# Optimization experiments

Hardware: AMD Instinct MI355X
Metric: run time of the kernel (lower is better)

Reference implementation:

```python
import jax, jax.numpy as jnp
import numpy as np

N = 500_000          # num nodes
K = 3                # neighbors per star subgraph = graphlet_size - 1
E = N * K            # one subgraph per node -> directed (center, nbr) edges
L = 2                # hop_neighbor
FD = 2               # final_dim = 2**pqc_dim
H = 64               # hidden_dim
NC = 8               # num_classes
NIN = 16             # node_input_dim
EIN = 8              # edge_input_dim


def _lin(k, i, o):
    # torch.nn.Linear-style init scale
    return jax.random.normal(k, (i, o), jnp.float32) * (1.0 / np.sqrt(i))


def setup_inputs() -> dict:
    key = jax.random.key(0)
    ks = jax.random.split(key, 32)
    node_feat = jax.random.normal(ks[0], (N, NIN), jnp.float32)
    edge_attr = jax.random.normal(ks[1], (E, EIN), jnp.float32)
    # edge e = (center, neighbor); centers grouped: edges 3i..3i+2 belong to node i
    centers = jnp.repeat(jnp.arange(N, dtype=jnp.int32), K)
    neighbors = jax.random.randint(ks[2], (E,), 0, N, dtype=jnp.int32)
    edge_index = jnp.stack([centers, neighbors])  # [2, E]
    batch = jnp.zeros((N,), jnp.int32)
    msg_W1 = jnp.stack([_lin(ks[6 + i], 2 * FD, H) for i in range(L)])
    msg_W2 = jnp.stack([_lin(ks[8 + i], H, FD) for i in range(L)])
    upd_W1 = jnp.stack([_lin(ks[10 + i], 2 * FD, H) for i in range(L)])
    upd_W2 = jnp.stack([_lin(ks[12 + i], H, FD) for i in range(L)])
    return dict(
        node_feat=node_feat, edge_attr=edge_attr, edge_index=edge_index, batch=batch,
        Wn=_lin(ks[3], NIN, FD), bn=jnp.zeros((FD,), jnp.float32),
        We=_lin(ks[4], EIN, FD), be=jnp.zeros((FD,), jnp.float32),
        msg_W1=msg_W1, msg_b1=jnp.zeros((L, H), jnp.float32),
        msg_W2=msg_W2, msg_b2=jnp.zeros((L, FD), jnp.float32),
        upd_W1=upd_W1, upd_b1=jnp.zeros((L, H), jnp.float32),
        upd_W2=upd_W2, upd_b2=jnp.zeros((L, FD), jnp.float32),
        fin_W1=_lin(ks[14], FD, H), fin_b1=jnp.zeros((H,), jnp.float32),
        fin_W2=_lin(ks[15], H, NC), fin_b2=jnp.zeros((NC,), jnp.float32),
    )


def _leaky(x):
    return jnp.where(x >= 0, x, 0.1 * x)


def _mlp(x, W1, b1, W2, b2):
    # MLP([din, 64, dout], act=LeakyReLU(0.1)); dropout inactive at eval
    return _leaky(x @ W1 + b1) @ W2 + b2


def reference(node_feat, edge_attr, edge_index, batch, Wn, bn, We, be,
              msg_W1, msg_b1, msg_W2, msg_b2, upd_W1, upd_b1, upd_W2, upd_b2,
              fin_W1, fin_b1, fin_W2, fin_b2):
    ctr = edge_index[0]  # [E] center of each star edge
    nbr = edge_index[1]  # [E] neighbor
    h = node_feat @ Wn + bn      # [N, FD] input_node projection
    e = edge_attr @ We + be      # [E, FD] input_edge projection (fixed across layers)
    for l in range(L):
        # message over each (center, neighbor) edge: concat(edge_feat, nbr_feat)
        msg = _mlp(jnp.concatenate([e, h[nbr]], axis=1),
                   msg_W1[l], msg_b1[l], msg_W2[l], msg_b2[l])  # [E, FD]
        aggr = jax.ops.segment_sum(msg, ctr, num_segments=N)    # [N, FD]
        new = _mlp(jnp.concatenate([h, aggr], axis=1),
                   upd_W1[l], upd_b1[l], upd_W2[l], upd_b2[l])  # [N, FD]
        h = jax.nn.relu(h + new)  # updates_node[center] += new_center; then ReLU
    return _mlp(h, fin_W1, fin_b1, fin_W2, fin_b2)  # [N, NC]
```

## Files before the change

### kernel.cpp

```cpp
#include <hip/hip_runtime.h>

#define NN 500000
#define HALF 250000
#define KK 3
#define EE (NN * KK)
#define HH 64
#define NC 8
#define NIN 16
#define EIN 8

typedef __attribute__((ext_vector_type(2))) _Float16 h2;
typedef __attribute__((ext_vector_type(2)))  float sf2;
typedef __attribute__((ext_vector_type(8)))  float sf8;
typedef __attribute__((ext_vector_type(16))) float sf16;

using pk_t = decltype(__builtin_amdgcn_cvt_pkrtz(0.f, 0.f));

__device__ __forceinline__ sf2 sload2(const float* p) {
    sf2 r; asm("s_load_dwordx2 %0, %1, 0x0" : "=s"(r) : "s"(p)); return r;
}
__device__ __forceinline__ sf8 sload8(const float* p) {
    sf8 r; asm("s_load_dwordx8 %0, %1, 0x0" : "=s"(r) : "s"(p)); return r;
}
__device__ __forceinline__ sf16 sload16(const float* p) {
    sf16 r; asm("s_load_dwordx16 %0, %1, 0x0" : "=s"(r) : "s"(p)); return r;
}
#define SWAIT1(a)         asm volatile("s_waitcnt lgkmcnt(0)" : "+s"(a))
#define SWAIT2(a,b)       asm volatile("s_waitcnt lgkmcnt(0)" : "+s"(a),"+s"(b))
#define SWAIT3(a,b,c)     asm volatile("s_waitcnt lgkmcnt(0)" : "+s"(a),"+s"(b),"+s"(c))
#define SWAIT4(a,b,c,d)   asm volatile("s_waitcnt lgkmcnt(0)" : "+s"(a),"+s"(b),"+s"(c),"+s"(d))
#define SWAIT5(a,b,c,d,e) asm volatile("s_waitcnt lgkmcnt(0)" : "+s"(a),"+s"(b),"+s"(c),"+s"(d),"+s"(e))

#if __has_builtin(__builtin_elementwise_fma)
#define PKFMA(a,b,c) __builtin_elementwise_fma((a),(b),(c))
#else
#define PKFMA(a,b,c) ((a)*(b)+(c))
#endif

__device__ __forceinline__ h2 bch2(float f)        { return __builtin_bit_cast(h2, f); }
__device__ __forceinline__ h2 bch2u(unsigned int u){ return __builtin_bit_cast(h2, u); }
__device__ __forceinline__ h2 dup16(float f) {
    return __builtin_bit_cast(h2, __builtin_amdgcn_cvt_pkrtz(f, f));
}
__device__ __forceinline__ unsigned int pkrtz_u(float a, float b) {
    return __builtin_bit_cast(unsigned int, __builtin_amdgcn_cvt_pkrtz(a, b));
}
__device__ __forceinline__ h2 splat_lo(unsigned int u) {
    h2 p = bch2u(u); h2 r; r.x = p.x; r.y = p.x; return r;
}
__device__ __forceinline__ h2 splat_hi(unsigned int u) {
    h2 p = bch2u(u); h2 r; r.x = p.y; r.y = p.y; return r;
}
__device__ __forceinline__ float lo_f32(unsigned int u) { return (float)bch2u(u).x; }
__device__ __forceinline__ float hi_f32(unsigned int u) { return (float)bch2u(u).y; }

__device__ __forceinline__ float fdot2(h2 a, h2 b, float c) {
#if __has_builtin(__builtin_amdgcn_fdot2)
    return __builtin_amdgcn_fdot2(__builtin_bit_cast(pk_t, a),
                                  __builtin_bit_cast(pk_t, b), c, false);
#else
    return c + (float)a.x * (float)b.x + (float)a.y * (float)b.y;
#endif
}
__device__ __forceinline__ h2 lk2(h2 x) {
    h2 c = {(_Float16)0.1f, (_Float16)0.1f};
    return __builtin_elementwise_max(x, x * c);
}
__device__ __forceinline__ float pack2(float a, float b) {
    h2 v; v.x = (_Float16)a; v.y = (_Float16)b;
    return __builtin_bit_cast(float, v);
}

__global__ __launch_bounds__(256) void prep_kernel(
    const float* __restrict__ node_feat, const float* __restrict__ edge_attr,
    const float* __restrict__ Wn, const float* __restrict__ bn,
    const float* __restrict__ We, const float* __restrict__ be,
    unsigned int* __restrict__ hp, unsigned int* __restrict__ ep,
    const float* __restrict__ msgW1, const float* __restrict__ msgb1, const float* __restrict__ msgW2,
    const float* __restrict__ updW1, const float* __restrict__ updb1, const float* __restrict__ updW2,
    const float* __restrict__ finW1, const float* __restrict__ finb1, const float* __restrict__ finW2,
    float* __restrict__ wpack)
{
    sf16 wn0 = sload16(Wn);
    sf16 wn1 = sload16(Wn + 16);
    sf2  bnv = sload2(bn);
    sf16 wev = sload16(We);
    sf2  bev = sload2(be);
    SWAIT5(wn0, wn1, bnv, wev, bev);

    int idx = blockIdx.x * 256 + threadIdx.x;
    if (idx < NN) {
        const float4* x4 = (const float4*)(node_feat + (size_t)idx * NIN);
        float4 v0 = x4[0], v1 = x4[1], v2 = x4[2], v3 = x4[3];
        float xs[16] = {v0.x, v0.y, v0.z, v0.w, v1.x, v1.y, v1.z, v1.w,
                        v2.x, v2.y, v2.z, v2.w, v3.x, v3.y, v3.z, v3.w};
        float a0 = bnv.x, a1 = bnv.y;
#pragma unroll
        for (int i = 0; i < 8; i++) {
            a0 = fmaf(xs[i], wn0[2 * i], a0);
            a1 = fmaf(xs[i], wn0[2 * i + 1], a1);
        }
#pragma unroll
        for (int i = 0; i < 8; i++) {
            a0 = fmaf(xs[8 + i], wn1[2 * i], a0);
            a1 = fmaf(xs[8 + i], wn1[2 * i + 1], a1);
        }
        hp[idx] = pkrtz_u(a0, a1);
    } else if (idx < NN + EE) {
        int eidx = idx - NN;
        const float4* x4 = (const float4*)(edge_attr + (size_t)eidx * EIN);
        float4 v0 = x4[0], v1 = x4[1];
        float xs[8] = {v0.x, v0.y, v0.z, v0.w, v1.x, v1.y, v1.z, v1.w};
        float a0 = bev.x, a1 = bev.y;
#pragma unroll
        for (int i = 0; i < 8; i++) {
            a0 = fmaf(xs[i], wev[2 * i], a0);
            a1 = fmaf(xs[i], wev[2 * i + 1], a1);
        }
        ep[eidx] = pkrtz_u(a0, a1);
    }

    if (blockIdx.x == 0) {
        int t = threadIdx.x;
        if (t < 32) {
            int l = t >> 4, which = (t >> 3) & 1, c = t & 7;
            const float* W1 = (which ? updW1 : msgW1) + l * 4 * HH;
            const float* b1 = (which ? updb1 : msgb1) + l * HH;
            const float* W2 = (which ? updW2 : msgW2) + l * 2 * HH;
            float* dst = wpack + (l * 2 + which) * 256 + c * 32;
            int j0 = c * 8;
            for (int r = 0; r < 4; r++)
                for (int p = 0; p < 4; p++)
                    dst[r * 4 + p] = pack2(W1[r * HH + j0 + 2 * p], W1[r * HH + j0 + 2 * p + 1]);
            for (int p = 0; p < 4; p++) {
                dst[16 + p] = pack2(b1[j0 + 2 * p], b1[j0 + 2 * p + 1]);
                dst[20 + p] = pack2(W2[(j0 + 2 * p) * 2 + 0], W2[(j0 + 2 * p + 1) * 2 + 0]);
                dst[24 + p] = pack2(W2[(j0 + 2 * p) * 2 + 1], W2[(j0 + 2 * p + 1) * 2 + 1]);
                dst[28 + p] = 0.0f;
            }
        } else if (t < 40) {
            int c = t - 32, j0 = c * 8;
            float* dst = wpack + 1024 + c * 48;
            for (int p = 0; p < 4; p++) {
                dst[p]      = pack2(finW1[j0 + 2 * p],      finW1[j0 + 2 * p + 1]);
                dst[4 + p]  = pack2(finW1[HH + j0 + 2 * p], finW1[HH + j0 + 2 * p + 1]);
                dst[8 + p]  = pack2(finb1[j0 + 2 * p],      finb1[j0 + 2 * p + 1]);
                dst[12 + p] = 0.0f;
            }
            for (int jp = 0; jp < 4; jp++)
                for (int cc = 0; cc < NC; cc++)
                    dst[16 + jp * 8 + cc] = pack2(finW2[(j0 + 2 * jp) * NC + cc],
                                                  finW2[(j0 + 2 * jp + 1) * NC + cc]);
        }
    }
}

template<bool FINAL>
__global__ __launch_bounds__(256) void layer_kernel(
    const unsigned int* __restrict__ hp_in, const unsigned int* __restrict__ eP,
    const int* __restrict__ nbr,
    const float* __restrict__ mblk, const float* __restrict__ mb2,
    const float* __restrict__ ublk, const float* __restrict__ ub2,
    unsigned int* __restrict__ hp_out,
    const float* __restrict__ fblk, const float* __restrict__ fb2,
    float* __restrict__ out)
{
    int tA = blockIdx.x * 256 + threadIdx.x;
    if (tA >= HALF) return;
    int iA = tA, iB = tA + HALF;

    sf2 mb2v = sload2(mb2);
    sf2 ub2v = sload2(ub2);
    SWAIT2(mb2v, ub2v);

    unsigned int hA = hp_in[iA], hB = hp_in[iB];
    int baseA = iA * KK, baseB = iB * KK;
    int nA0 = nbr[baseA], nA1 = nbr[baseA + 1], nA2 = nbr[baseA + 2];
    int nB0 = nbr[baseB], nB1 = nbr[baseB + 1], nB2 = nbr[baseB + 2];
    unsigned int gA0 = hp_in[nA0], gA1 = hp_in[nA1], gA2 = hp_in[nA2];
    unsigned int gB0 = hp_in[nB0], gB1 = hp_in[nB1], gB2 = hp_in[nB2];
    unsigned int eA0 = eP[baseA], eA1 = eP[baseA + 1], eA2 = eP[baseA + 2];
    unsigned int eB0 = eP[baseB], eB1 = eP[baseB + 1], eB2 = eP[baseB + 2];

    h2 eA0x = splat_lo(eA0), eA0y = splat_hi(eA0);
    h2 eA1x = splat_lo(eA1), eA1y = splat_hi(eA1);
    h2 eA2x = splat_lo(eA2), eA2y = splat_hi(eA2);
    h2 eB0x = splat_lo(eB0), eB0y = splat_hi(eB0);
    h2 eB1x = splat_lo(eB1), eB1y = splat_hi(eB1);
    h2 eB2x = splat_lo(eB2), eB2y = splat_hi(eB2);
    h2 nA0x = splat_lo(gA0), nA0y = splat_hi(gA0);
    h2 nA1x = splat_lo(gA1), nA1y = splat_hi(gA1);
    h2 nA2x = splat_lo(gA2), nA2y = splat_hi(gA2);
    h2 nB0x = splat_lo(gB0), nB0y = splat_hi(gB0);
    h2 nB1x = splat_lo(gB1), nB1y = splat_hi(gB1);
    h2 nB2x = splat_lo(gB2), nB2y = splat_hi(gB2);

    float a0A = 3.0f * mb2v.x, a1A = 3.0f * mb2v.y;
    float a0B = a0A, a1B = a1A;
#pragma unroll 1
    for (int c = 0; c < 8; c += 2) {
        sf16 A0 = sload16(mblk + c * 32);
        sf16 B0 = sload16(mblk + c * 32 + 16);
        sf16 A1 = sload16(mblk + c * 32 + 32);
        sf16 B1 = sload16(mblk + c * 32 + 48);
        SWAIT4(A0, B0, A1, B1);
#pragma unroll
        for (int half = 0; half < 2; half++) {
            const sf16& A = half ? A1 : A0;
            const sf16& B = half ? B1 : B0;
#pragma unroll
            for (int jp = 0; jp < 4; jp++) {
                h2 w0 = bch2(A[jp]), w1 = bch2(A[4 + jp]);
                h2 w2 = bch2(A[8 + jp]), w3 = bch2(A[12 + jp]);
                h2 bb = bch2(B[jp]);
                h2 wcx = bch2(B[4 + jp]), wcy = bch2(B[8 + jp]);
                h2 t0 = PKFMA(eA0x, w0, PKFMA(eA0y, w1, PKFMA(nA0x, w2, PKFMA(nA0y, w3, bb))));
                h2 t1 = PKFMA(eA1x, w0, PKFMA(eA1y, w1, PKFMA(nA1x, w2, PKFMA(nA1y, w3, bb))));
                h2 t2 = PKFMA(eA2x, w0, PKFMA(eA2y, w1, PKFMA(nA2x, w2, PKFMA(nA2y, w3, bb))));
                h2 tsA = lk2(t0) + lk2(t1) + lk2(t2);
                a0A = fdot2(tsA, wcx, a0A);
                a1A = fdot2(tsA, wcy, a1A);
                h2 s0 = PKFMA(eB0x, w0, PKFMA(eB0y, w1, PKFMA(nB0x, w2, PKFMA(nB0y, w3, bb))));
                h2 s1 = PKFMA(eB1x, w0, PKFMA(eB1y, w1, PKFMA(nB1x, w2, PKFMA(nB1y, w3, bb))));
                h2 s2 = PKFMA(eB2x, w0, PKFMA(eB2y, w1, PKFMA(nB2x, w2, PKFMA(nB2y, w3, bb))));
                h2 tsB = lk2(s0) + lk2(s1) + lk2(s2);
                a0B = fdot2(tsB, wcx, a0B);
                a1B = fdot2(tsB, wcy, a1B);
            }
        }
    }

    h2 hAx = splat_lo(hA), hAy = splat_hi(hA);
    h2 hBx = splat_lo(hB), hBy = splat_hi(hB);
    h2 aAx = dup16(a0A), aAy = dup16(a1A);
    h2 aBx = dup16(a0B), aBy = dup16(a1B);
    float u0A = ub2v.x, u1A = ub2v.y, u0B = ub2v.x, u1B = ub2v.y;
#pragma unroll 1
    for (int c = 0; c < 8; c += 2) {
        sf16 A0 = sload16(ublk + c * 32);
        sf16 B0 = sload16(ublk + c * 32 + 16);
        sf16 A1 = sload16(ublk + c * 32 + 32);
        sf16 B1 = sload16(ublk + c * 32 + 48);
        SWAIT4(A0, B0, A1, B1);
#pragma unroll
        for (int half = 0; half < 2; half++) {
            const sf16& A = half ? A1 : A0;
            const sf16& B = half ? B1 : B0;
#pragma unroll
            for (int jp = 0; jp < 4; jp++) {
                h2 w0 = bch2(A[jp]), w1 = bch2(A[4 + jp]);
                h2 w2 = bch2(A[8 + jp]), w3 = bch2(A[12 + jp]);
                h2 bb = bch2(B[jp]);
                h2 wcx = bch2(B[4 + jp]), wcy = bch2(B[8 + jp]);
                h2 tt = PKFMA(hAx, w0, PKFMA(hAy, w1, PKFMA(aAx, w2, PKFMA(aAy, w3, bb))));
                tt = lk2(tt);
                u0A = fdot2(tt, wcx, u0A);
                u1A = fdot2(tt, wcy, u1A);
                h2 ss = PKFMA(hBx, w0, PKFMA(hBy, w1, PKFMA(aBx, w2, PKFMA(aBy, w3, bb))));
                ss = lk2(ss);
                u0B = fdot2(ss, wcx, u0B);
                u1B = fdot2(ss, wcy, u1B);
            }
        }
    }
    float nhA0 = fmaxf(lo_f32(hA) + u0A, 0.0f);
    float nhA1 = fmaxf(hi_f32(hA) + u1A, 0.0f);
    float nhB0 = fmaxf(lo_f32(hB) + u0B, 0.0f);
    float nhB1 = fmaxf(hi_f32(hB) + u1B, 0.0f);

    if constexpr (!FINAL) {
        hp_out[iA] = pkrtz_u(nhA0, nhA1);
        hp_out[iB] = pkrtz_u(nhB0, nhB1);
    } else {
        sf8 fb2v = sload8(fb2);
        SWAIT1(fb2v);
        float oA[NC], oB[NC];
#pragma unroll
        for (int cc = 0; cc < NC; cc++) { oA[cc] = fb2v[cc]; oB[cc] = fb2v[cc]; }
        h2 nAx = dup16(nhA0), nAy = dup16(nhA1);
        h2 nBx = dup16(nhB0), nBy = dup16(nhB1);
#pragma unroll 1
        for (int c = 0; c < 8; c++) {
            sf16 A = sload16(fblk + c * 48);
            sf16 B = sload16(fblk + c * 48 + 16);
            sf16 C = sload16(fblk + c * 48 + 32);
            SWAIT3(A, B, C);
#pragma unroll
            for (int jp = 0; jp < 4; jp++) {
                h2 w1a = bch2(A[jp]), w1b = bch2(A[4 + jp]), bb = bch2(A[8 + jp]);
                h2 ttA = lk2(PKFMA(nAx, w1a, PKFMA(nAy, w1b, bb)));
                h2 ttB = lk2(PKFMA(nBx, w1a, PKFMA(nBy, w1b, bb)));
#pragma unroll
                for (int cc = 0; cc < NC; cc++) {
                    float w = (jp < 2) ? B[(jp & 1) * 8 + cc] : C[(jp & 1) * 8 + cc];
                    h2 wv = bch2(w);
                    oA[cc] = fdot2(ttA, wv, oA[cc]);
                    oB[cc] = fdot2(ttB, wv, oB[cc]);
                }
            }
        }
        float4* opA = (float4*)(out + (size_t)iA * NC);
        opA[0] = make_float4(oA[0], oA[1], oA[2], oA[3]);
        opA[1] = make_float4(oA[4], oA[5], oA[6], oA[7]);
        float4* opB = (float4*)(out + (size_t)iB * NC);
        opB[0] = make_float4(oB[0], oB[1], oB[2], oB[3]);
        opB[1] = make_float4(oB[4], oB[5], oB[6], oB[7]);
    }
}

extern "C" void kernel_launch(void* const* d_in, const int* in_sizes, int n_in,
                              void* d_out, int out_size, void* d_ws, size_t ws_size,
                              hipStream_t stream) {
    const float* node_feat = (const float*)d_in[0];
    const float* edge_attr = (const float*)d_in[1];
    const int* edge_index = (const int*)d_in[2];
    const float* Wn = (const float*)d_in[4];
    const float* bn = (const float*)d_in[5];
    const float* We = (const float*)d_in[6];
    const float* be = (const float*)d_in[7];
    const float* msgW1 = (const float*)d_in[8];
    const float* msgb1 = (const float*)d_in[9];
    const float* msgW2 = (const float*)d_in[10];
    const float* msgb2 = (const float*)d_in[11];
    const float* updW1 = (const float*)d_in[12];
    const float* updb1 = (const float*)d_in[13];
    const float* updW2 = (const float*)d_in[14];
    const float* updb2 = (const float*)d_in[15];
    const float* finW1 = (const float*)d_in[16];
    const float* finb1 = (const float*)d_in[17];
    const float* finW2 = (const float*)d_in[18];
    const float* finb2 = (const float*)d_in[19];
    float* out = (float*)d_out;

    const int* nbr = edge_index + EE;

    char* ws = (char*)d_ws;
    unsigned int* hA = (unsigned int*)ws;
    unsigned int* hB = (unsigned int*)(ws + (size_t)NN * 4);
    unsigned int* eP = (unsigned int*)(ws + (size_t)NN * 8);
    float* wpack = (float*)(ws + (size_t)NN * 8 + (size_t)EE * 4);

    const int threads = 256;
    int prep_grid = (NN + EE + threads - 1) / threads;
    prep_kernel<<<prep_grid, threads, 0, stream>>>(
        node_feat, edge_attr, Wn, bn, We, be, hA, eP,
        msgW1, msgb1, msgW2, updW1, updb1, updW2,
        finW1, finb1, finW2, wpack);

    int grid = (HALF + threads - 1) / threads;
    layer_kernel<false><<<grid, threads, 0, stream>>>(
        hA, eP, nbr,
        wpack + 0 * 256, msgb2,
        wpack + 1 * 256, updb2,
        hB, wpack + 1024, finb2, nullptr);
    layer_kernel<true><<<grid, threads, 0, stream>>>(
        hB, eP, nbr,
        wpack + 2 * 256, msgb2 + 2,
        wpack + 3 * 256, updb2 + 2,
        nullptr, wpack + 1024, finb2, out);
}
```

Before: 198.4 us.

## Fuse prep and both layers into one cooperative kernel with grid syncs

Replaces the three launches (prep plus two layer kernels) with a single cooperative kernel of 512 blocks that uses grid.sync between phases. Each thread now handles four nodes, and it keeps its edge projections and neighbor indices in registers across layers, so the projected edge buffer is never written to or reread from global memory. This removes launch gaps and edge-buffer traffic. In exchange it adds grid-wide barriers, much higher register pressure from four nodes per thread, and fewer threads to hide the latency of the random gathers.

```diff
diff --git a/kernel.cpp b/kernel.cpp
--- a/kernel.cpp
+++ b/kernel.cpp
@@ -1,13 +1,18 @@
 #include <hip/hip_runtime.h>
+#include <hip/hip_cooperative_groups.h>
+
+namespace cg = cooperative_groups;
 
 #define NN 500000
-#define HALF 250000
+#define QTR 125000
 #define KK 3
 #define EE (NN * KK)
 #define HH 64
 #define NC 8
 #define NIN 16
 #define EIN 8
+#define TPB 256
+#define NBLK 512
 
 typedef __attribute__((ext_vector_type(2))) _Float16 h2;
 typedef __attribute__((ext_vector_type(2)))  float sf2;
@@ -71,63 +76,207 @@
     return __builtin_bit_cast(float, v);
 }
 
-__global__ __launch_bounds__(256) void prep_kernel(
-    const float* __restrict__ node_feat, const float* __restrict__ edge_attr,
-    const float* __restrict__ Wn, const float* __restrict__ bn,
-    const float* __restrict__ We, const float* __restrict__ be,
-    unsigned int* __restrict__ hp, unsigned int* __restrict__ ep,
-    const float* __restrict__ msgW1, const float* __restrict__ msgb1, const float* __restrict__ msgW2,
-    const float* __restrict__ updW1, const float* __restrict__ updb1, const float* __restrict__ updW2,
-    const float* __restrict__ finW1, const float* __restrict__ finb1, const float* __restrict__ finW2,
-    float* __restrict__ wpack)
+struct KParams {
+    const float* node_feat; const float* edge_attr; const int* nbr;
+    const float* Wn; const float* bn; const float* We; const float* be;
+    const float* msgW1; const float* msgb1; const float* msgW2; const float* msgb2;
+    const float* updW1; const float* updb1; const float* updW2; const float* updb2;
+    const float* finW1; const float* finb1; const float* finW2; const float* finb2;
+    unsigned int* hbufA; unsigned int* hbufB; float* wpack; float* out;
+};
+
+__device__ __forceinline__ unsigned int proj_node(const float* node_feat, int idx,
+                                                  const sf16& wn0, const sf16& wn1,
+                                                  const sf2& bnv) {
+    const float4* x4 = (const float4*)(node_feat + (size_t)idx * NIN);
+    float4 v0 = x4[0], v1 = x4[1], v2 = x4[2], v3 = x4[3];
+    float xs[16] = {v0.x, v0.y, v0.z, v0.w, v1.x, v1.y, v1.z, v1.w,
+                    v2.x, v2.y, v2.z, v2.w, v3.x, v3.y, v3.z, v3.w};
+    float a0 = bnv.x, a1 = bnv.y;
+#pragma unroll
+    for (int i = 0; i < 8; i++) {
+        a0 = fmaf(xs[i], wn0[2 * i], a0);
+        a1 = fmaf(xs[i], wn0[2 * i + 1], a1);
+    }
+#pragma unroll
+    for (int i = 0; i < 8; i++) {
+        a0 = fmaf(xs[8 + i], wn1[2 * i], a0);
+        a1 = fmaf(xs[8 + i], wn1[2 * i + 1], a1);
+    }
+    return pkrtz_u(a0, a1);
+}
+
+__device__ __forceinline__ unsigned int proj_edge(const float* edge_attr, int eidx,
+                                                  const sf16& wev, const sf2& bev) {
+    const float4* x4 = (const float4*)(edge_attr + (size_t)eidx * EIN);
+    float4 v0 = x4[0], v1 = x4[1];
+    float xs[8] = {v0.x, v0.y, v0.z, v0.w, v1.x, v1.y, v1.z, v1.w};
+    float a0 = bev.x, a1 = bev.y;
+#pragma unroll
+    for (int i = 0; i < 8; i++) {
+        a0 = fmaf(xs[i], wev[2 * i], a0);
+        a1 = fmaf(xs[i], wev[2 * i + 1], a1);
+    }
+    return pkrtz_u(a0, a1);
+}
+
+template<bool FINAL>
+__device__ __forceinline__ void layer_phase(
+    const KParams& P, int l, const int* idx,
+    const unsigned int* h, const int* nb, const unsigned int* ee,
+    const unsigned int* __restrict__ hp_in, unsigned int* nh)
 {
-    sf16 wn0 = sload16(Wn);
-    sf16 wn1 = sload16(Wn + 16);
-    sf2  bnv = sload2(bn);
-    sf16 wev = sload16(We);
-    sf2  bev = sload2(be);
-    SWAIT5(wn0, wn1, bnv, wev, bev);
-
-    int idx = blockIdx.x * 256 + threadIdx.x;
-    if (idx < NN) {
-        const float4* x4 = (const float4*)(node_feat + (size_t)idx * NIN);
-        float4 v0 = x4[0], v1 = x4[1], v2 = x4[2], v3 = x4[3];
-        float xs[16] = {v0.x, v0.y, v0.z, v0.w, v1.x, v1.y, v1.z, v1.w,
-                        v2.x, v2.y, v2.z, v2.w, v3.x, v3.y, v3.z, v3.w};
-        float a0 = bnv.x, a1 = bnv.y;
-#pragma unroll
-        for (int i = 0; i < 8; i++) {
-            a0 = fmaf(xs[i], wn0[2 * i], a0);
-            a1 = fmaf(xs[i], wn0[2 * i + 1], a1);
-        }
-#pragma unroll
-        for (int i = 0; i < 8; i++) {
-            a0 = fmaf(xs[8 + i], wn1[2 * i], a0);
-            a1 = fmaf(xs[8 + i], wn1[2 * i + 1], a1);
-        }
-        hp[idx] = pkrtz_u(a0, a1);
-    } else if (idx < NN + EE) {
-        int eidx = idx - NN;
-        const float4* x4 = (const float4*)(edge_attr + (size_t)eidx * EIN);
-        float4 v0 = x4[0], v1 = x4[1];
-        float xs[8] = {v0.x, v0.y, v0.z, v0.w, v1.x, v1.y, v1.z, v1.w};
-        float a0 = bev.x, a1 = bev.y;
-#pragma unroll
-        for (int i = 0; i < 8; i++) {
-            a0 = fmaf(xs[i], wev[2 * i], a0);
-            a1 = fmaf(xs[i], wev[2 * i + 1], a1);
-        }
-        ep[eidx] = pkrtz_u(a0, a1);
-    }
+    const float* mblk = P.wpack + (2 * l) * 256;
+    const float* ublk = P.wpack + (2 * l + 1) * 256;
+    sf2 mb2v = sload2(P.msgb2 + 2 * l);
+    sf2 ub2v = sload2(P.updb2 + 2 * l);
+    SWAIT2(mb2v, ub2v);
+
+    h2 ex[12], ey[12], gx[12], gy[12];
+#pragma unroll
+    for (int k = 0; k < 12; k++) {
+        unsigned int g = hp_in[nb[k]];
+        ex[k] = splat_lo(ee[k]); ey[k] = splat_hi(ee[k]);
+        gx[k] = splat_lo(g);     gy[k] = splat_hi(g);
+    }
+
+    float a0[4], a1[4];
+#pragma unroll
+    for (int n = 0; n < 4; n++) { a0[n] = 3.0f * mb2v.x; a1[n] = 3.0f * mb2v.y; }
+#pragma unroll 1
+    for (int c = 0; c < 8; c += 2) {
+        sf16 A0 = sload16(mblk + c * 32);
+        sf16 B0 = sload16(mblk + c * 32 + 16);
+        sf16 A1 = sload16(mblk + c * 32 + 32);
+        sf16 B1 = sload16(mblk + c * 32 + 48);
+        SWAIT4(A0, B0, A1, B1);
+#pragma unroll
+        for (int half = 0; half < 2; half++) {
+            const sf16& A = half ? A1 : A0;
+            const sf16& B = half ? B1 : B0;
+#pragma unroll
+            for (int jp = 0; jp < 4; jp++) {
+                h2 w0 = bch2(A[jp]), w1 = bch2(A[4 + jp]);
+                h2 w2 = bch2(A[8 + jp]), w3 = bch2(A[12 + jp]);
+                h2 bb = bch2(B[jp]);
+                h2 wcx = bch2(B[4 + jp]), wcy = bch2(B[8 + jp]);
+#pragma unroll
+                for (int n = 0; n < 4; n++) {
+                    int k = 3 * n;
+                    h2 t0 = PKFMA(ex[k],     w0, PKFMA(ey[k],     w1, PKFMA(gx[k],     w2, PKFMA(gy[k],     w3, bb))));
+                    h2 t1 = PKFMA(ex[k + 1], w0, PKFMA(ey[k + 1], w1, PKFMA(gx[k + 1], w2, PKFMA(gy[k + 1], w3, bb))));
+                    h2 t2 = PKFMA(ex[k + 2], w0, PKFMA(ey[k + 2], w1, PKFMA(gx[k + 2], w2, PKFMA(gy[k + 2], w3, bb))));
+                    h2 ts = lk2(t0) + lk2(t1) + lk2(t2);
+                    a0[n] = fdot2(ts, wcx, a0[n]);
+                    a1[n] = fdot2(ts, wcy, a1[n]);
+                }
+            }
+        }
+    }
+
+    h2 hx[4], hy[4], ax[4], ay[4];
+#pragma unroll
+    for (int n = 0; n < 4; n++) {
+        hx[n] = splat_lo(h[n]); hy[n] = splat_hi(h[n]);
+        ax[n] = dup16(a0[n]);   ay[n] = dup16(a1[n]);
+    }
+    float u0[4], u1[4];
+#pragma unroll
+    for (int n = 0; n < 4; n++) { u0[n] = ub2v.x; u1[n] = ub2v.y; }
+#pragma unroll 1
+    for (int c = 0; c < 8; c += 2) {
+        sf16 A0 = sload16(ublk + c * 32);
+        sf16 B0 = sload16(ublk + c * 32 + 16);
+        sf16 A1 = sload16(ublk + c * 32 + 32);
+        sf16 B1 = sload16(ublk + c * 32 + 48);
+        SWAIT4(A0, B0, A1, B1);
+#pragma unroll
+        for (int half = 0; half < 2; half++) {
+            const sf16& A = half ? A1 : A0;
+            const sf16& B = half ? B1 : B0;
+#pragma unroll
+            for (int jp = 0; jp < 4; jp++) {
+                h2 w0 = bch2(A[jp]), w1 = bch2(A[4 + jp]);
+                h2 w2 = bch2(A[8 + jp]), w3 = bch2(A[12 + jp]);
+                h2 bb = bch2(B[jp]);
+                h2 wcx = bch2(B[4 + jp]), wcy = bch2(B[8 + jp]);
+#pragma unroll
+                for (int n = 0; n < 4; n++) {
+                    h2 tt = PKFMA(hx[n], w0, PKFMA(hy[n], w1, PKFMA(ax[n], w2, PKFMA(ay[n], w3, bb))));
+                    tt = lk2(tt);
+                    u0[n] = fdot2(tt, wcx, u0[n]);
+                    u1[n] = fdot2(tt, wcy, u1[n]);
+                }
+            }
+        }
+    }
+    float nh0[4], nh1[4];
+#pragma unroll
+    for (int n = 0; n < 4; n++) {
+        nh0[n] = fmaxf(lo_f32(h[n]) + u0[n], 0.0f);
+        nh1[n] = fmaxf(hi_f32(h[n]) + u1[n], 0.0f);
+        nh[n] = pkrtz_u(nh0[n], nh1[n]);
+    }
+
+    if constexpr (FINAL) {
+        const float* fblk = P.wpack + 1024;
+        sf8 fb2v = sload8(P.finb2);
+        SWAIT1(fb2v);
+        float o[4][NC];
+#pragma unroll
+        for (int n = 0; n < 4; n++)
+#pragma unroll
+            for (int cc = 0; cc < NC; cc++) o[n][cc] = fb2v[cc];
+        h2 nx[4], ny[4];
+#pragma unroll
+        for (int n = 0; n < 4; n++) { nx[n] = dup16(nh0[n]); ny[n] = dup16(nh1[n]); }
+#pragma unroll 1
+        for (int c = 0; c < 8; c++) {
+            sf16 A = sload16(fblk + c * 48);
+            sf16 B = sload16(fblk + c * 48 + 16);
+            sf16 C = sload16(fblk + c * 48 + 32);
+            SWAIT3(A, B, C);
+#pragma unroll
+            for (int jp = 0; jp < 4; jp++) {
+                h2 w1a = bch2(A[jp]), w1b = bch2(A[4 + jp]), bb = bch2(A[8 + jp]);
+                h2 tt[4];
+#pragma unroll
+                for (int n = 0; n < 4; n++)
+                    tt[n] = lk2(PKFMA(nx[n], w1a, PKFMA(ny[n], w1b, bb)));
+#pragma unroll
+                for (int cc = 0; cc < NC; cc++) {
+                    float w = (jp < 2) ? B[(jp & 1) * 8 + cc] : C[(jp & 1) * 8 + cc];
+                    h2 wv = bch2(w);
+#pragma unroll
+                    for (int n = 0; n < 4; n++) o[n][cc] = fdot2(tt[n], wv, o[n][cc]);
+                }
+            }
+        }
+#pragma unroll
+        for (int n = 0; n < 4; n++) {
+            float4* op = (float4*)(P.out + (size_t)idx[n] * NC);
+            op[0] = make_float4(o[n][0], o[n][1], o[n][2], o[n][3]);
+            op[1] = make_float4(o[n][4], o[n][5], o[n][6], o[n][7]);
+        }
+    }
+}
+
+__global__ __launch_bounds__(TPB, 2) void fused_kernel(KParams P) {
+    cg::grid_group grid = cg::this_grid();
+    const int t = blockIdx.x * TPB + threadIdx.x;
+    const bool active = (t < QTR);
+    int idx[4];
+#pragma unroll
+    for (int n = 0; n < 4; n++) idx[n] = t + n * QTR;
 
     if (blockIdx.x == 0) {
-        int t = threadIdx.x;
-        if (t < 32) {
-            int l = t >> 4, which = (t >> 3) & 1, c = t & 7;
-            const float* W1 = (which ? updW1 : msgW1) + l * 4 * HH;
-            const float* b1 = (which ? updb1 : msgb1) + l * HH;
-            const float* W2 = (which ? updW2 : msgW2) + l * 2 * HH;
-            float* dst = wpack + (l * 2 + which) * 256 + c * 32;
+        int tt = threadIdx.x;
+        if (tt < 32) {
+            int l = tt >> 4, which = (tt >> 3) & 1, c = tt & 7;
+            const float* W1 = (which ? P.updW1 : P.msgW1) + l * 4 * HH;
+            const float* b1 = (which ? P.updb1 : P.msgb1) + l * HH;
+            const float* W2 = (which ? P.updW2 : P.msgW2) + l * 2 * HH;
+            float* dst = P.wpack + (l * 2 + which) * 256 + c * 32;
             int j0 = c * 8;
             for (int r = 0; r < 4; r++)
                 for (int p = 0; p < 4; p++)
@@ -138,224 +287,82 @@
                 dst[24 + p] = pack2(W2[(j0 + 2 * p) * 2 + 1], W2[(j0 + 2 * p + 1) * 2 + 1]);
                 dst[28 + p] = 0.0f;
             }
-        } else if (t < 40) {
-            int c = t - 32, j0 = c * 8;
-            float* dst = wpack + 1024 + c * 48;
+        } else if (tt < 40) {
+            int c = tt - 32, j0 = c * 8;
+            float* dst = P.wpack + 1024 + c * 48;
             for (int p = 0; p < 4; p++) {
-                dst[p]      = pack2(finW1[j0 + 2 * p],      finW1[j0 + 2 * p + 1]);
-                dst[4 + p]  = pack2(finW1[HH + j0 + 2 * p], finW1[HH + j0 + 2 * p + 1]);
-                dst[8 + p]  = pack2(finb1[j0 + 2 * p],      finb1[j0 + 2 * p + 1]);
+                dst[p]      = pack2(P.finW1[j0 + 2 * p],      P.finW1[j0 + 2 * p + 1]);
+                dst[4 + p]  = pack2(P.finW1[HH + j0 + 2 * p], P.finW1[HH + j0 + 2 * p + 1]);
+                dst[8 + p]  = pack2(P.finb1[j0 + 2 * p],      P.finb1[j0 + 2 * p + 1]);
                 dst[12 + p] = 0.0f;
             }
             for (int jp = 0; jp < 4; jp++)
                 for (int cc = 0; cc < NC; cc++)
-                    dst[16 + jp * 8 + cc] = pack2(finW2[(j0 + 2 * jp) * NC + cc],
-                                                  finW2[(j0 + 2 * jp + 1) * NC + cc]);
-        }
-    }
-}
-
-template<bool FINAL>
-__global__ __launch_bounds__(256) void layer_kernel(
-    const unsigned int* __restrict__ hp_in, const unsigned int* __restrict__ eP,
-    const int* __restrict__ nbr,
-    const float* __restrict__ mblk, const float* __restrict__ mb2,
-    const float* __restrict__ ublk, const float* __restrict__ ub2,
-    unsigned int* __restrict__ hp_out,
-    const float* __restrict__ fblk, const float* __restrict__ fb2,
-    float* __restrict__ out)
-{
-    int tA = blockIdx.x * 256 + threadIdx.x;
-    if (tA >= HALF) return;
-    int iA = tA, iB = tA + HALF;
-
-    sf2 mb2v = sload2(mb2);
-    sf2 ub2v = sload2(ub2);
-    SWAIT2(mb2v, ub2v);
-
-    unsigned int hA = hp_in[iA], hB = hp_in[iB];
-    int baseA = iA * KK, baseB = iB * KK;
-    int nA0 = nbr[baseA], nA1 = nbr[baseA + 1], nA2 = nbr[baseA + 2];
-    int nB0 = nbr[baseB], nB1 = nbr[baseB + 1], nB2 = nbr[baseB + 2];
-    unsigned int gA0 = hp_in[nA0], gA1 = hp_in[nA1], gA2 = hp_in[nA2];
-    unsigned int gB0 = hp_in[nB0], gB1 = hp_in[nB1], gB2 = hp_in[nB2];
-    unsigned int eA0 = eP[baseA], eA1 = eP[baseA + 1], eA2 = eP[baseA + 2];
-    unsigned int eB0 = eP[baseB], eB1 = eP[baseB + 1], eB2 = eP[baseB + 2];
-
-    h2 eA0x = splat_lo(eA0), eA0y = splat_hi(eA0);
-    h2 eA1x = splat_lo(eA1), eA1y = splat_hi(eA1);
-    h2 eA2x = splat_lo(eA2), eA2y = splat_hi(eA2);
-    h2 eB0x = splat_lo(eB0), eB0y = splat_hi(eB0);
-    h2 eB1x = splat_lo(eB1), eB1y = splat_hi(eB1);
-    h2 eB2x = splat_lo(eB2), eB2y = splat_hi(eB2);
-    h2 nA0x = splat_lo(gA0), nA0y = splat_hi(gA0);
-    h2 nA1x = splat_lo(gA1), nA1y = splat_hi(gA1);
-    h2 nA2x = splat_lo(gA2), nA2y = splat_hi(gA2);
-    h2 nB0x = splat_lo(gB0), nB0y = splat_hi(gB0);
-    h2 nB1x = splat_lo(gB1), nB1y = splat_hi(gB1);
-    h2 nB2x = splat_lo(gB2), nB2y = splat_hi(gB2);
-
-    float a0A = 3.0f * mb2v.x, a1A = 3.0f * mb2v.y;
-    float a0B = a0A, a1B = a1A;
-#pragma unroll 1
-    for (int c = 0; c < 8; c += 2) {
-        sf16 A0 = sload16(mblk + c * 32);
-        sf16 B0 = sload16(mblk + c * 32 + 16);
-        sf16 A1 = sload16(mblk + c * 32 + 32);
-        sf16 B1 = sload16(mblk + c * 32 + 48);
-        SWAIT4(A0, B0, A1, B1);
-#pragma unroll
-        for (int half = 0; half < 2; half++) {
-            const sf16& A = half ? A1 : A0;
-            const sf16& B = half ? B1 : B0;
-#pragma unroll
-            for (int jp = 0; jp < 4; jp++) {
-                h2 w0 = bch2(A[jp]), w1 = bch2(A[4 + jp]);
-                h2 w2 = bch2(A[8 + jp]), w3 = bch2(A[12 + jp]);
-                h2 bb = bch2(B[jp]);
-                h2 wcx = bch2(B[4 + jp]), wcy = bch2(B[8 + jp]);
-                h2 t0 = PKFMA(eA0x, w0, PKFMA(eA0y, w1, PKFMA(nA0x, w2, PKFMA(nA0y, w3, bb))));
-                h2 t1 = PKFMA(eA1x, w0, PKFMA(eA1y, w1, PKFMA(nA1x, w2, PKFMA(nA1y, w3, bb))));
-                h2 t2 = PKFMA(eA2x, w0, PKFMA(eA2y, w1, PKFMA(nA2x, w2, PKFMA(nA2y, w3, bb))));
-                h2 tsA = lk2(t0) + lk2(t1) + lk2(t2);
-                a0A = fdot2(tsA, wcx, a0A);
-                a1A = fdot2(tsA, wcy, a1A);
-                h2 s0 = PKFMA(eB0x, w0, PKFMA(eB0y, w1, PKFMA(nB0x, w2, PKFMA(nB0y, w3, bb))));
-                h2 s1 = PKFMA(eB1x, w0, PKFMA(eB1y, w1, PKFMA(nB1x, w2, PKFMA(nB1y, w3, bb))));
-                h2 s2 = PKFMA(eB2x, w0, PKFMA(eB2y, w1, PKFMA(nB2x, w2, PKFMA(nB2y, w3, bb))));
-                h2 tsB = lk2(s0) + lk2(s1) + lk2(s2);
-                a0B = fdot2(tsB, wcx, a0B);
-                a1B = fdot2(tsB, wcy, a1B);
-            }
-        }
-    }
-
-    h2 hAx = splat_lo(hA), hAy = splat_hi(hA);
-    h2 hBx = splat_lo(hB), hBy = splat_hi(hB);
-    h2 aAx = dup16(a0A), aAy = dup16(a1A);
-    h2 aBx = dup16(a0B), aBy = dup16(a1B);
-    float u0A = ub2v.x, u1A = ub2v.y, u0B = ub2v.x, u1B = ub2v.y;
-#pragma unroll 1
-    for (int c = 0; c < 8; c += 2) {
-        sf16 A0 = sload16(ublk + c * 32);
-        sf16 B0 = sload16(ublk + c * 32 + 16);
-        sf16 A1 = sload16(ublk + c * 32 + 32);
-        sf16 B1 = sload16(ublk + c * 32 + 48);
-        SWAIT4(A0, B0, A1, B1);
-#pragma unroll
-        for (int half = 0; half < 2; half++) {
-            const sf16& A = half ? A1 : A0;
-            const sf16& B = half ? B1 : B0;
-#pragma unroll
-            for (int jp = 0; jp < 4; jp++) {
-                h2 w0 = bch2(A[jp]), w1 = bch2(A[4 + jp]);
-                h2 w2 = bch2(A[8 + jp]), w3 = bch2(A[12 + jp]);
-                h2 bb = bch2(B[jp]);
-                h2 wcx = bch2(B[4 + jp]), wcy = bch2(B[8 + jp]);
-                h2 tt = PKFMA(hAx, w0, PKFMA(hAy, w1, PKFMA(aAx, w2, PKFMA(aAy, w3, bb))));
-                tt = lk2(tt);
-                u0A = fdot2(tt, wcx, u0A);
-                u1A = fdot2(tt, wcy, u1A);
-                h2 ss = PKFMA(hBx, w0, PKFMA(hBy, w1, PKFMA(aBx, w2, PKFMA(aBy, w3, bb))));
-                ss = lk2(ss);
-                u0B = fdot2(ss, wcx, u0B);
-                u1B = fdot2(ss, wcy, u1B);
-            }
-        }
-    }
-    float nhA0 = fmaxf(lo_f32(hA) + u0A, 0.0f);
-    float nhA1 = fmaxf(hi_f32(hA) + u1A, 0.0f);
-    float nhB0 = fmaxf(lo_f32(hB) + u0B, 0.0f);
-    float nhB1 = fmaxf(hi_f32(hB) + u1B, 0.0f);
-
-    if constexpr (!FINAL) {
-        hp_out[iA] = pkrtz_u(nhA0, nhA1);
-        hp_out[iB] = pkrtz_u(nhB0, nhB1);
-    } else {
-        sf8 fb2v = sload8(fb2);
-        SWAIT1(fb2v);
-        float oA[NC], oB[NC];
-#pragma unroll
-        for (int cc = 0; cc < NC; cc++) { oA[cc] = fb2v[cc]; oB[cc] = fb2v[cc]; }
-        h2 nAx = dup16(nhA0), nAy = dup16(nhA1);
-        h2 nBx = dup16(nhB0), nBy = dup16(nhB1);
-#pragma unroll 1
-        for (int c = 0; c < 8; c++) {
-            sf16 A = sload16(fblk + c * 48);
-            sf16 B = sload16(fblk + c * 48 + 16);
-            sf16 C = sload16(fblk + c * 48 + 32);
-            SWAIT3(A, B, C);
-#pragma unroll
-            for (int jp = 0; jp < 4; jp++) {
-                h2 w1a = bch2(A[jp]), w1b = bch2(A[4 + jp]), bb = bch2(A[8 + jp]);
-                h2 ttA = lk2(PKFMA(nAx, w1a, PKFMA(nAy, w1b, bb)));
-                h2 ttB = lk2(PKFMA(nBx, w1a, PKFMA(nBy, w1b, bb)));
-#pragma unroll
-                for (int cc = 0; cc < NC; cc++) {
-                    float w = (jp < 2) ? B[(jp & 1) * 8 + cc] : C[(jp & 1) * 8 + cc];
-                    h2 wv = bch2(w);
-                    oA[cc] = fdot2(ttA, wv, oA[cc]);
-                    oB[cc] = fdot2(ttB, wv, oB[cc]);
-                }
-            }
-        }
-        float4* opA = (float4*)(out + (size_t)iA * NC);
-        opA[0] = make_float4(oA[0], oA[1], oA[2], oA[3]);
-        opA[1] = make_float4(oA[4], oA[5], oA[6], oA[7]);
-        float4* opB = (float4*)(out + (size_t)iB * NC);
-        opB[0] = make_float4(oB[0], oB[1], oB[2], oB[3]);
-        opB[1] = make_float4(oB[4], oB[5], oB[6], oB[7]);
+                    dst[16 + jp * 8 + cc] = pack2(P.finW2[(j0 + 2 * jp) * NC + cc],
+                                                  P.finW2[(j0 + 2 * jp + 1) * NC + cc]);
+        }
+    }
+
+    unsigned int h[4] = {0, 0, 0, 0};
+    unsigned int ee[12] = {0};
+    int nb[12] = {0};
+    if (active) {
+        sf16 wn0 = sload16(P.Wn);
+        sf16 wn1 = sload16(P.Wn + 16);
+        sf2  bnv = sload2(P.bn);
+        sf16 wev = sload16(P.We);
+        sf2  bev = sload2(P.be);
+        SWAIT5(wn0, wn1, bnv, wev, bev);
+#pragma unroll
+        for (int n = 0; n < 4; n++) {
+            h[n] = proj_node(P.node_feat, idx[n], wn0, wn1, bnv);
+            P.hbufA[idx[n]] = h[n];
+#pragma unroll
+            for (int k = 0; k < 3; k++) {
+                ee[3 * n + k] = proj_edge(P.edge_attr, idx[n] * KK + k, wev, bev);
+                nb[3 * n + k] = P.nbr[idx[n] * KK + k];
+            }
+        }
+    }
+    grid.sync();
+
+    unsigned int nh[4] = {0, 0, 0, 0};
+    if (active) {
+        layer_phase<false>(P, 0, idx, h, nb, ee, P.hbufA, nh);
+#pragma unroll
+        for (int n = 0; n < 4; n++) P.hbufB[idx[n]] = nh[n];
+    }
+    grid.sync();
+
+    if (active) {
+        unsigned int dd[4];
+        layer_phase<true>(P, 1, idx, nh, nb, ee, P.hbufB, dd);
     }
 }
 
 extern "C" void kernel_launch(void* const* d_in, const int* in_sizes, int n_in,
                               void* d_out, int out_size, void* d_ws, size_t ws_size,
                               hipStream_t stream) {
-    const float* node_feat = (const float*)d_in[0];
-    const float* edge_attr = (const float*)d_in[1];
-    const int* edge_index = (const int*)d_in[2];
-    const float* Wn = (const float*)d_in[4];
-    const float* bn = (const float*)d_in[5];
-    const float* We = (const float*)d_in[6];
-    const float* be = (const float*)d_in[7];
-    const float* msgW1 = (const float*)d_in[8];
-    const float* msgb1 = (const float*)d_in[9];
-    const float* msgW2 = (const float*)d_in[10];
-    const float* msgb2 = (const float*)d_in[11];
-    const float* updW1 = (const float*)d_in[12];
-    const float* updb1 = (const float*)d_in[13];
-    const float* updW2 = (const float*)d_in[14];
-    const float* updb2 = (const float*)d_in[15];
-    const float* finW1 = (const float*)d_in[16];
-    const float* finb1 = (const float*)d_in[17];
-    const float* finW2 = (const float*)d_in[18];
-    const float* finb2 = (const float*)d_in[19];
-    float* out = (float*)d_out;
-
-    const int* nbr = edge_index + EE;
+    KParams P;
+    P.node_feat = (const float*)d_in[0];
+    P.edge_attr = (const float*)d_in[1];
+    P.nbr = ((const int*)d_in[2]) + EE;
+    P.Wn = (const float*)d_in[4];  P.bn = (const float*)d_in[5];
+    P.We = (const float*)d_in[6];  P.be = (const float*)d_in[7];
+    P.msgW1 = (const float*)d_in[8];  P.msgb1 = (const float*)d_in[9];
+    P.msgW2 = (const float*)d_in[10]; P.msgb2 = (const float*)d_in[11];
+    P.updW1 = (const float*)d_in[12]; P.updb1 = (const float*)d_in[13];
+    P.updW2 = (const float*)d_in[14]; P.updb2 = (const float*)d_in[15];
+    P.finW1 = (const float*)d_in[16]; P.finb1 = (const float*)d_in[17];
+    P.finW2 = (const float*)d_in[18]; P.finb2 = (const float*)d_in[19];
+    P.out = (float*)d_out;
 
     char* ws = (char*)d_ws;
-    unsigned int* hA = (unsigned int*)ws;
-    unsigned int* hB = (unsigned int*)(ws + (size_t)NN * 4);
-    unsigned int* eP = (unsigned int*)(ws + (size_t)NN * 8);
-    float* wpack = (float*)(ws + (size_t)NN * 8 + (size_t)EE * 4);
-
-    const int threads = 256;
-    int prep_grid = (NN + EE + threads - 1) / threads;
-    prep_kernel<<<prep_grid, threads, 0, stream>>>(
-        node_feat, edge_attr, Wn, bn, We, be, hA, eP,
-        msgW1, msgb1, msgW2, updW1, updb1, updW2,
-        finW1, finb1, finW2, wpack);
-
-    int grid = (HALF + threads - 1) / threads;
-    layer_kernel<false><<<grid, threads, 0, stream>>>(
-        hA, eP, nbr,
-        wpack + 0 * 256, msgb2,
-        wpack + 1 * 256, updb2,
-        hB, wpack + 1024, finb2, nullptr);
-    layer_kernel<true><<<grid, threads, 0, stream>>>(
-        hB, eP, nbr,
-        wpack + 2 * 256, msgb2 + 2,
-        wpack + 3 * 256, updb2 + 2,
-        nullptr, wpack + 1024, finb2, out);
-}
+    P.hbufA = (unsigned int*)ws;
+    P.hbufB = (unsigned int*)(ws + (size_t)NN * 4);
+    P.wpack = (float*)(ws + (size_t)NN * 8);
+
+    void* args[] = { (void*)&P };
+    hipLaunchCooperativeKernel((const void*)fused_kernel,
+                               dim3(NBLK), dim3(TPB), args, 0, stream);
+}
```

New measurement: 357.0 us. 1.8x slower.
